# Performance work log

Hardware: AMD Instinct MI355X
Metric: run time of the kernel (lower is better)

Reference implementation:

```python
import jax, jax.numpy as jnp
import numpy as np

B, T, C, H = 4, 4096, 1024, 64

def setup_inputs() -> dict:
    key = jax.random.key(0)
    kx, kq, kk, kv = jax.random.split(key, 4)
    x  = jax.random.normal(kx, (B, T, C), dtype=jnp.float32)
    # nn.Linear(C, H, bias=False) weights have shape [H, C]; y = x @ W.T
    Wq = jax.random.normal(kq, (H, C), dtype=jnp.float32) * (C ** -0.5)
    Wk = jax.random.normal(kk, (H, C), dtype=jnp.float32) * (C ** -0.5)
    Wv = jax.random.normal(kv, (H, C), dtype=jnp.float32) * (C ** -0.5)
    return {"x": x, "Wq": Wq, "Wk": Wk, "Wv": Wv}

def reference(x, Wq, Wk, Wv):
    T_ = x.shape[1]
    scale = jnp.asarray(Wq.shape[0] ** -0.5, dtype=x.dtype)
    q = jnp.einsum('btc,hc->bth', x, Wq)
    k = jnp.einsum('btc,hc->bth', x, Wk)
    v = jnp.einsum('btc,hc->bth', x, Wv)
    w = jnp.einsum('bqh,bkh->bqk', q, k)  # [B, T, T] scores
    causal = jnp.tril(jnp.ones((T_, T_), dtype=bool))
    # original: masked_fill(-inf) then scale; -inf * scale == -inf, so equivalent
    w = jnp.where(causal, w * scale, -jnp.inf)
    w = jax.nn.softmax(w, axis=-1)
    # dropout p=0.0 (eval/deterministic): identity
    return jnp.einsum('bqk,bkh->bqh', w, v)
```

## Files before the change

kernel.cpp:

```cpp
#include <hip/hip_runtime.h>
#include <hip/hip_bf16.h>

#define B_ 4
#define T_ 4096
#define C_ 1024

typedef __bf16 bf16_t;
typedef __bf16 bf16x8 __attribute__((ext_vector_type(8)));
typedef float f32x4 __attribute__((ext_vector_type(4)));

__device__ __forceinline__ void gld16(const void* g, void* l) {
    __builtin_amdgcn_global_load_lds((const __attribute__((address_space(1))) void*)g,
                                     (__attribute__((address_space(3))) void*)l, 16, 0, 0);
}

__global__ void wcvt_kernel(const float* __restrict__ Wq, const float* __restrict__ Wk,
                            const float* __restrict__ Wv, bf16_t* __restrict__ wbf) {
    int i = blockIdx.x * 256 + threadIdx.x;
    int m = i >> 16;
    int r = i & 65535;
    const float* src = (m == 0) ? Wq : (m == 1) ? Wk : Wv;
    float s = (m == 0) ? 0.125f * 1.44269504f : 1.0f;
    wbf[i] = (bf16_t)(src[r] * s);
}

__global__ __launch_bounds__(512, 4)
void qkv_proj_kernel(const float* __restrict__ x, const bf16_t* __restrict__ wbf,
                     bf16_t* __restrict__ qb, bf16_t* __restrict__ kb,
                     bf16_t* __restrict__ vtb) {
    __shared__ float  xs[3][2048];
    __shared__ bf16_t wsb[2][12288];

    const int tid = threadIdx.x;
    const int w = tid >> 6, lane = tid & 63, lr = lane & 15, kg = lane >> 4;
    const int rg = w & 1, cg = w >> 1;
    const int row0 = blockIdx.x * 32;

    const int xr0 = tid >> 4, xu = tid & 15;
    const char* xg = (const char*)x + (size_t)(row0 + xr0) * 4096
                     + ((xu ^ (xr0 & 15)) * 16);
    const int wh = tid >> 3, wu = tid & 7;
    const char* wg = (const char*)wbf;

    char* xs_c  = (char*)&xs[0][0];
    char* xs_n  = (char*)&xs[1][0];
    char* xs_nn = (char*)&xs[2][0];
    char* ws_c  = (char*)&wsb[0][0];
    char* ws_n  = (char*)&wsb[1][0];

#define ISSUE_X(kk, dst) {                                                          \
        gld16(xg + (size_t)(kk) * 256, (dst) + (size_t)tid * 16); }
#define ISSUE_W(kk, dst) {                                                          \
        _Pragma("unroll")                                                           \
        for (int j = 0; j < 3; ++j) {                                               \
            int h = wh + j * 64;                                                    \
            gld16(wg + (size_t)h * 2048 + (size_t)(kk) * 128 + ((wu ^ (h & 7)) * 16), \
                  (dst) + (size_t)(tid + j * 512) * 16); } }

    f32x4 acc[3];
    #pragma unroll
    for (int j = 0; j < 3; ++j) acc[j] = (f32x4){0.f, 0.f, 0.f, 0.f};

    ISSUE_X(0, xs_c);
    ISSUE_W(0, ws_c);
    ISSUE_X(1, xs_n);

    const int rl = rg * 16 + lr;
    const int u00 = ((2 * kg)     ^ lr) * 16;
    const int u01 = ((2 * kg + 1) ^ lr) * 16;
    const int u10 = ((2 * kg + 8) ^ lr) * 16;
    const int u11 = ((2 * kg + 9) ^ lr) * 16;

    #pragma clang loop unroll(disable)
    for (int c = 0; c < 16; ++c) {
        if (c < 15) {
            asm volatile("s_waitcnt vmcnt(1)" ::: "memory");
        } else {
            asm volatile("s_waitcnt vmcnt(0)" ::: "memory");
        }
        __builtin_amdgcn_s_barrier();
        if (c < 15) ISSUE_W(c + 1, ws_n);
        if (c < 14) ISSUE_X(c + 2, xs_nn);

        {
            const char* xrow = xs_c + (size_t)rl * 256;
            float4 a0 = *(const float4*)(xrow + u00);
            float4 a1 = *(const float4*)(xrow + u01);
            float4 b0 = *(const float4*)(xrow + u10);
            float4 b1 = *(const float4*)(xrow + u11);
            bf16x8 af0, af1;
            af0[0]=(bf16_t)a0.x; af0[1]=(bf16_t)a0.y; af0[2]=(bf16_t)a0.z; af0[3]=(bf16_t)a0.w;
            af0[4]=(bf16_t)a1.x; af0[5]=(bf16_t)a1.y; af0[6]=(bf16_t)a1.z; af0[7]=(bf16_t)a1.w;
            af1[0]=(bf16_t)b0.x; af1[1]=(bf16_t)b0.y; af1[2]=(bf16_t)b0.z; af1[3]=(bf16_t)b0.w;
            af1[4]=(bf16_t)b1.x; af1[5]=(bf16_t)b1.y; af1[6]=(bf16_t)b1.z; af1[7]=(bf16_t)b1.w;

            __builtin_amdgcn_s_setprio(1);
            #pragma unroll
            for (int j = 0; j < 3; ++j) {
                int h = (cg * 3 + j) * 16 + lr;
                const char* wrow = ws_c + (size_t)h * 128;
                bf16x8 w0 = *(const bf16x8*)(wrow + (((kg)     ^ (lr & 7)) * 16));
                bf16x8 w1 = *(const bf16x8*)(wrow + (((kg + 4) ^ (lr & 7)) * 16));
                acc[j] = __builtin_amdgcn_mfma_f32_16x16x32_bf16(af0, w0, acc[j], 0, 0, 0);
                acc[j] = __builtin_amdgcn_mfma_f32_16x16x32_bf16(af1, w1, acc[j], 0, 0, 0);
            }
            __builtin_amdgcn_s_setprio(0);
        }

        char* tx = xs_c; xs_c = xs_n; xs_n = xs_nn; xs_nn = tx;
        char* tw = ws_c; ws_c = ws_n; ws_n = tw;
    }

    #pragma unroll
    for (int j = 0; j < 3; ++j) {
        int p = cg * 3 + j;
        int m = p >> 2;
        int h = (p & 3) * 16 + lr;
        #pragma unroll
        for (int i = 0; i < 4; ++i) {
            int t = row0 + rg * 16 + kg * 4 + i;
            float v = acc[j][i];
            if (m == 0) {
                qb[(size_t)t * 64 + h] = (bf16_t)v;
            } else if (m == 1) {
                kb[(size_t)t * 64 + ((((h >> 3) ^ (t & 7)) << 3) | (h & 7))] = (bf16_t)v;
            } else {
                int bb = t >> 12, tt = t & 4095;
                vtb[(size_t)(bb * 64 + h) * 4096 + (tt & ~63)
                    + (((((tt >> 3) & 7) ^ (h & 7))) << 3) + (tt & 7)] = (bf16_t)v;
            }
        }
    }
#undef ISSUE_X
#undef ISSUE_W
}

__global__ __launch_bounds__(256, 2)
void attn_kernel(const bf16_t* __restrict__ qb, const bf16_t* __restrict__ kb,
                 const bf16_t* __restrict__ vtb, float* __restrict__ out) {
    __shared__ bf16_t kvb[2][2][8192];
    __shared__ bf16_t p_lds[4][16][68];

    const int tid = threadIdx.x;
    const int w = tid >> 6, lane = tid & 63, lr = lane & 15, kg = lane >> 4;
    const int rg = w & 1, slice = w >> 1;
    const int bid = blockIdx.x;
    const int b = bid & 3;
    const int qt = 127 - (bid >> 2);
    const int qrow0 = qt * 32 + rg * 16;
    const size_t bT = (size_t)b * 4096;

    const int nch    = (qt + 2) >> 1;
    const int nsteps = (nch + 1) >> 1;

#define STAGE_CHUNK(kk, pp, cc) {                                                   \
        _Pragma("unroll")                                                           \
        for (int jj = 0; jj < 2; ++jj) {                                            \
            int idx = tid + jj * 256;                                               \
            gld16((const char*)kb + (bT + (size_t)(kk) * 64) * 128 + (size_t)idx * 16, \
                  (char*)&kvb[pp][cc][0] + (size_t)idx * 16);                       \
            gld16((const char*)vtb + (size_t)(b * 64 + (idx >> 3)) * 8192           \
                      + (size_t)(kk) * 128 + (idx & 7) * 16,                        \
                  (char*)&kvb[pp][cc][4096] + (size_t)idx * 16); } }
#define STAGE_PAIR(j1) {                                                            \
        int c0 = 2 * (j1), c1 = 2 * (j1) + 1, pp = (j1) & 1;                        \
        if (c0 < nch) STAGE_CHUNK(c0, pp, 0);                                       \
        if (c1 < nch) STAGE_CHUNK(c1, pp, 1); }

    bf16x8 qf[2];
    #pragma unroll
    for (int s = 0; s < 2; ++s)
        qf[s] = *(const bf16x8*)&qb[(bT + qrow0 + lr) * 64 + s * 32 + kg * 8];

    f32x4 o_acc[4];
    float l_i[4];
    #pragma unroll
    for (int ct = 0; ct < 4; ++ct) o_acc[ct] = (f32x4){0.f, 0.f, 0.f, 0.f};
    #pragma unroll
    for (int i = 0; i < 4; ++i) l_i[i] = 0.f;

    STAGE_PAIR(0);

    for (int j = 0; j < nsteps; ++j) {
        asm volatile("s_waitcnt vmcnt(0)" ::: "memory");
        __builtin_amdgcn_s_barrier();
        asm volatile("" ::: "memory");
        if (j + 1 < nsteps) STAGE_PAIR(j + 1);

        int c = 2 * j + slice;
        if (c < nch) {
            const bf16_t* Kt = &kvb[j & 1][slice][0];
            const bf16_t* Vt = &kvb[j & 1][slice][4096];
            int kv0 = c * 64;

            f32x4 sc[4];
            #pragma unroll
            for (int ct = 0; ct < 4; ++ct) sc[ct] = (f32x4){0.f, 0.f, 0.f, 0.f};
            __builtin_amdgcn_s_setprio(1);
            #pragma unroll
            for (int ct = 0; ct < 4; ++ct)
                #pragma unroll
                for (int s = 0; s < 2; ++s) {
                    bf16x8 kf = *(const bf16x8*)&Kt[(ct * 16 + lr) * 64 + (((kg + 4 * s) ^ (lr & 7)) * 8)];
                    sc[ct] = __builtin_amdgcn_mfma_f32_16x16x32_bf16(qf[s], kf, sc[ct], 0, 0, 0);
                }
            __builtin_amdgcn_s_setprio(0);

            if (kv0 + 63 > qrow0) {
                #pragma unroll
                for (int ct = 0; ct < 4; ++ct)
                    #pragma unroll
                    for (int i = 0; i < 4; ++i) {
                        int col = kv0 + ct * 16 + lr;
                        int rw  = qrow0 + kg * 4 + i;
                        if (col > rw) sc[ct][i] = -INFINITY;
                    }
            }

            #pragma unroll
            for (int ct = 0; ct < 4; ++ct)
                #pragma unroll
                for (int i = 0; i < 4; ++i) {
                    float p = __builtin_amdgcn_exp2f(sc[ct][i]);
                    p_lds[w][kg * 4 + i][ct * 16 + lr] = (bf16_t)p;
                    l_i[i] += p;
                }

            bf16x8 pf[2];
            #pragma unroll
            for (int s = 0; s < 2; ++s)
                pf[s] = *(const bf16x8*)&p_lds[w][lr][s * 32 + kg * 8];
            __builtin_amdgcn_s_setprio(1);
            #pragma unroll
            for (int ct = 0; ct < 4; ++ct)
                #pragma unroll
                for (int s = 0; s < 2; ++s) {
                    bf16x8 vf = *(const bf16x8*)&Vt[(ct * 16 + lr) * 64 + (((kg + 4 * s) ^ (lr & 7)) * 8)];
                    o_acc[ct] = __builtin_amdgcn_mfma_f32_16x16x32_bf16(pf[s], vf, o_acc[ct], 0, 0, 0);
                }
            __builtin_amdgcn_s_setprio(0);
        }
    }

    asm volatile("s_waitcnt vmcnt(0)" ::: "memory");
    __syncthreads();

    #pragma unroll
    for (int off = 1; off < 16; off <<= 1)
        #pragma unroll
        for (int i = 0; i < 4; ++i)
            l_i[i] += __shfl_xor(l_i[i], off);

    float* co = (float*)&kvb[0][0][0];
    float* cl = co + 2 * 16 * 66;
    if (slice == 1) {
        #pragma unroll
        for (int ct = 0; ct < 4; ++ct)
            #pragma unroll
            for (int i = 0; i < 4; ++i)
                co[(rg * 16 + kg * 4 + i) * 66 + ct * 16 + lr] = o_acc[ct][i];
        if (lr == 0) {
            #pragma unroll
            for (int i = 0; i < 4; ++i)
                cl[rg * 16 + kg * 4 + i] = l_i[i];
        }
    }
    __syncthreads();
    if (slice == 0) {
        #pragma unroll
        for (int i = 0; i < 4; ++i) {
            int r = kg * 4 + i;
            float lv = l_i[i] + cl[rg * 16 + r];
            float inv = 1.0f / lv;
            #pragma unroll
            for (int ct = 0; ct < 4; ++ct) {
                float ov = o_acc[ct][i] + co[(rg * 16 + r) * 66 + ct * 16 + lr];
                out[(bT + qrow0 + r) * 64 + ct * 16 + lr] = ov * inv;
            }
        }
    }
#undef STAGE_CHUNK
#undef STAGE_PAIR
}

extern "C" void kernel_launch(void* const* d_in, const int* in_sizes, int n_in,
                              void* d_out, int out_size, void* d_ws, size_t ws_size,
                              hipStream_t stream) {
    const float* x  = (const float*)d_in[0];
    const float* Wq = (const float*)d_in[1];
    const float* Wk = (const float*)d_in[2];
    const float* Wv = (const float*)d_in[3];
    float* out = (float*)d_out;

    bf16_t* ws  = (bf16_t*)d_ws;
    bf16_t* wbf = ws;
    bf16_t* qb  = ws + 196608;
    bf16_t* kb  = qb + 1048576;
    bf16_t* vtb = kb + 1048576;

    wcvt_kernel<<<768, 256, 0, stream>>>(Wq, Wk, Wv, wbf);
    qkv_proj_kernel<<<512, 512, 0, stream>>>(x, wbf, qb, kb, vtb);
    attn_kernel<<<512, 256, 0, stream>>>(qb, kb, vtb, out);
}
```

Measured before the change: 62.41 us.

## Split attention KV range four ways per 64-row query tile with separate combine kernel

The attention kernel now assigns each block a 64-row query tile (four waves of 16 rows) and one quarter of its causal KV chunk range. Each block writes partial outputs and row sums to workspace, and a new combine kernel adds the four partials and normalises. The KV staging becomes a three-buffer ring that waits on vmcnt(4), keeping one chunk in flight during compute instead of the old paired double buffer. This removes the intra-block slice reduction and evens out per-block work, at the cost of 64 MB of extra partial-output traffic and one more kernel launch.

```diff
diff --git a/kernel.cpp b/kernel.cpp
--- a/kernel.cpp
+++ b/kernel.cpp
@@ -137,40 +137,44 @@
 
 __global__ __launch_bounds__(256, 2)
 void attn_kernel(const bf16_t* __restrict__ qb, const bf16_t* __restrict__ kb,
-                 const bf16_t* __restrict__ vtb, float* __restrict__ out) {
-    __shared__ bf16_t kvb[2][2][8192];
+                 const bf16_t* __restrict__ vtb, float* __restrict__ po,
+                 float* __restrict__ pl) {
+    __shared__ bf16_t kvb[3][8192];
     __shared__ bf16_t p_lds[4][16][68];
 
     const int tid = threadIdx.x;
     const int w = tid >> 6, lane = tid & 63, lr = lane & 15, kg = lane >> 4;
-    const int rg = w & 1, slice = w >> 1;
     const int bid = blockIdx.x;
     const int b = bid & 3;
-    const int qt = 127 - (bid >> 2);
-    const int qrow0 = qt * 32 + rg * 16;
+    const int v = bid >> 2;
+    const int s = v & 3;
+    const int qt = 63 - (v >> 2);
+    const int qrow0 = qt * 64 + w * 16;
     const size_t bT = (size_t)b * 4096;
 
-    const int nch    = (qt + 2) >> 1;
-    const int nsteps = (nch + 1) >> 1;
-
-#define STAGE_CHUNK(kk, pp, cc) {                                                   \
+    const int nch   = qt + 1;
+    const int start = (nch * s) >> 2;
+    const int end   = (nch * (s + 1)) >> 2;
+    const int cnt   = end - start;
+
+    char* ks_c  = (char*)&kvb[0][0];
+    char* ks_n  = (char*)&kvb[1][0];
+    char* ks_nn = (char*)&kvb[2][0];
+
+#define STAGE_CHUNK(kk, dst) {                                                      \
         _Pragma("unroll")                                                           \
         for (int jj = 0; jj < 2; ++jj) {                                            \
             int idx = tid + jj * 256;                                               \
             gld16((const char*)kb + (bT + (size_t)(kk) * 64) * 128 + (size_t)idx * 16, \
-                  (char*)&kvb[pp][cc][0] + (size_t)idx * 16);                       \
+                  (dst) + (size_t)idx * 16);                                        \
             gld16((const char*)vtb + (size_t)(b * 64 + (idx >> 3)) * 8192           \
                       + (size_t)(kk) * 128 + (idx & 7) * 16,                        \
-                  (char*)&kvb[pp][cc][4096] + (size_t)idx * 16); } }
-#define STAGE_PAIR(j1) {                                                            \
-        int c0 = 2 * (j1), c1 = 2 * (j1) + 1, pp = (j1) & 1;                        \
-        if (c0 < nch) STAGE_CHUNK(c0, pp, 0);                                       \
-        if (c1 < nch) STAGE_CHUNK(c1, pp, 1); }
+                  (dst) + 8192 + (size_t)idx * 16); } }
 
     bf16x8 qf[2];
     #pragma unroll
-    for (int s = 0; s < 2; ++s)
-        qf[s] = *(const bf16x8*)&qb[(bT + qrow0 + lr) * 64 + s * 32 + kg * 8];
+    for (int s2 = 0; s2 < 2; ++s2)
+        qf[s2] = *(const bf16x8*)&qb[(bT + qrow0 + lr) * 64 + s2 * 32 + kg * 8];
 
     f32x4 o_acc[4];
     float l_i[4];
@@ -179,71 +183,73 @@
     #pragma unroll
     for (int i = 0; i < 4; ++i) l_i[i] = 0.f;
 
-    STAGE_PAIR(0);
-
-    for (int j = 0; j < nsteps; ++j) {
-        asm volatile("s_waitcnt vmcnt(0)" ::: "memory");
+    if (cnt > 0) STAGE_CHUNK(start, ks_c);
+    if (cnt > 1) STAGE_CHUNK(start + 1, ks_n);
+
+    for (int j = 0; j < cnt; ++j) {
+        if (j < cnt - 1) {
+            asm volatile("s_waitcnt vmcnt(4)" ::: "memory");
+        } else {
+            asm volatile("s_waitcnt vmcnt(0)" ::: "memory");
+        }
         __builtin_amdgcn_s_barrier();
         asm volatile("" ::: "memory");
-        if (j + 1 < nsteps) STAGE_PAIR(j + 1);
-
-        int c = 2 * j + slice;
-        if (c < nch) {
-            const bf16_t* Kt = &kvb[j & 1][slice][0];
-            const bf16_t* Vt = &kvb[j & 1][slice][4096];
-            int kv0 = c * 64;
-
-            f32x4 sc[4];
-            #pragma unroll
-            for (int ct = 0; ct < 4; ++ct) sc[ct] = (f32x4){0.f, 0.f, 0.f, 0.f};
-            __builtin_amdgcn_s_setprio(1);
-            #pragma unroll
-            for (int ct = 0; ct < 4; ++ct)
-                #pragma unroll
-                for (int s = 0; s < 2; ++s) {
-                    bf16x8 kf = *(const bf16x8*)&Kt[(ct * 16 + lr) * 64 + (((kg + 4 * s) ^ (lr & 7)) * 8)];
-                    sc[ct] = __builtin_amdgcn_mfma_f32_16x16x32_bf16(qf[s], kf, sc[ct], 0, 0, 0);
-                }
-            __builtin_amdgcn_s_setprio(0);
-
-            if (kv0 + 63 > qrow0) {
-                #pragma unroll
-                for (int ct = 0; ct < 4; ++ct)
-                    #pragma unroll
-                    for (int i = 0; i < 4; ++i) {
-                        int col = kv0 + ct * 16 + lr;
-                        int rw  = qrow0 + kg * 4 + i;
-                        if (col > rw) sc[ct][i] = -INFINITY;
-                    }
-            }
-
+        if (j + 2 < cnt) STAGE_CHUNK(start + j + 2, ks_nn);
+
+        const bf16_t* Kt = (const bf16_t*)ks_c;
+        const bf16_t* Vt = (const bf16_t*)(ks_c + 8192);
+        const int c = start + j;
+        const int kv0 = c * 64;
+
+        f32x4 sc[4];
+        #pragma unroll
+        for (int ct = 0; ct < 4; ++ct) sc[ct] = (f32x4){0.f, 0.f, 0.f, 0.f};
+        __builtin_amdgcn_s_setprio(1);
+        #pragma unroll
+        for (int ct = 0; ct < 4; ++ct)
+            #pragma unroll
+            for (int s2 = 0; s2 < 2; ++s2) {
+                bf16x8 kf = *(const bf16x8*)&Kt[(ct * 16 + lr) * 64 + (((kg + 4 * s2) ^ (lr & 7)) * 8)];
+                sc[ct] = __builtin_amdgcn_mfma_f32_16x16x32_bf16(qf[s2], kf, sc[ct], 0, 0, 0);
+            }
+        __builtin_amdgcn_s_setprio(0);
+
+        if (c == nch - 1) {
             #pragma unroll
             for (int ct = 0; ct < 4; ++ct)
                 #pragma unroll
                 for (int i = 0; i < 4; ++i) {
-                    float p = __builtin_amdgcn_exp2f(sc[ct][i]);
-                    p_lds[w][kg * 4 + i][ct * 16 + lr] = (bf16_t)p;
-                    l_i[i] += p;
+                    int col = kv0 + ct * 16 + lr;
+                    int rw  = qrow0 + kg * 4 + i;
+                    if (col > rw) sc[ct][i] = -INFINITY;
                 }
-
-            bf16x8 pf[2];
-            #pragma unroll
-            for (int s = 0; s < 2; ++s)
-                pf[s] = *(const bf16x8*)&p_lds[w][lr][s * 32 + kg * 8];
-            __builtin_amdgcn_s_setprio(1);
-            #pragma unroll
-            for (int ct = 0; ct < 4; ++ct)
-                #pragma unroll
-                for (int s = 0; s < 2; ++s) {
-                    bf16x8 vf = *(const bf16x8*)&Vt[(ct * 16 + lr) * 64 + (((kg + 4 * s) ^ (lr & 7)) * 8)];
-                    o_acc[ct] = __builtin_amdgcn_mfma_f32_16x16x32_bf16(pf[s], vf, o_acc[ct], 0, 0, 0);
-                }
-            __builtin_amdgcn_s_setprio(0);
-        }
+        }
+
+        #pragma unroll
+        for (int ct = 0; ct < 4; ++ct)
+            #pragma unroll
+            for (int i = 0; i < 4; ++i) {
+                float p = __builtin_amdgcn_exp2f(sc[ct][i]);
+                p_lds[w][kg * 4 + i][ct * 16 + lr] = (bf16_t)p;
+                l_i[i] += p;
+            }
+
+        bf16x8 pf[2];
+        #pragma unroll
+        for (int s2 = 0; s2 < 2; ++s2)
+            pf[s2] = *(const bf16x8*)&p_lds[w][lr][s2 * 32 + kg * 8];
+        __builtin_amdgcn_s_setprio(1);
+        #pragma unroll
+        for (int ct = 0; ct < 4; ++ct)
+            #pragma unroll
+            for (int s2 = 0; s2 < 2; ++s2) {
+                bf16x8 vf = *(const bf16x8*)&Vt[(ct * 16 + lr) * 64 + (((kg + 4 * s2) ^ (lr & 7)) * 8)];
+                o_acc[ct] = __builtin_amdgcn_mfma_f32_16x16x32_bf16(pf[s2], vf, o_acc[ct], 0, 0, 0);
+            }
+        __builtin_amdgcn_s_setprio(0);
+
+        char* t0 = ks_c; ks_c = ks_n; ks_n = ks_nn; ks_nn = t0;
     }
-
-    asm volatile("s_waitcnt vmcnt(0)" ::: "memory");
-    __syncthreads();
 
     #pragma unroll
     for (int off = 1; off < 16; off <<= 1)
@@ -251,36 +257,27 @@
         for (int i = 0; i < 4; ++i)
             l_i[i] += __shfl_xor(l_i[i], off);
 
-    float* co = (float*)&kvb[0][0][0];
-    float* cl = co + 2 * 16 * 66;
-    if (slice == 1) {
+    const size_t pbase = ((size_t)s * 4 + b) * 4096;
+    #pragma unroll
+    for (int i = 0; i < 4; ++i) {
+        int row = qt * 64 + w * 16 + kg * 4 + i;
         #pragma unroll
         for (int ct = 0; ct < 4; ++ct)
-            #pragma unroll
-            for (int i = 0; i < 4; ++i)
-                co[(rg * 16 + kg * 4 + i) * 66 + ct * 16 + lr] = o_acc[ct][i];
-        if (lr == 0) {
-            #pragma unroll
-            for (int i = 0; i < 4; ++i)
-                cl[rg * 16 + kg * 4 + i] = l_i[i];
-        }
-    }
-    __syncthreads();
-    if (slice == 0) {
-        #pragma unroll
-        for (int i = 0; i < 4; ++i) {
-            int r = kg * 4 + i;
-            float lv = l_i[i] + cl[rg * 16 + r];
-            float inv = 1.0f / lv;
-            #pragma unroll
-            for (int ct = 0; ct < 4; ++ct) {
-                float ov = o_acc[ct][i] + co[(rg * 16 + r) * 66 + ct * 16 + lr];
-                out[(bT + qrow0 + r) * 64 + ct * 16 + lr] = ov * inv;
-            }
-        }
+            po[(pbase + row) * 64 + ct * 16 + lr] = o_acc[ct][i];
+        if (lr == 0) pl[pbase + row] = l_i[i];
     }
 #undef STAGE_CHUNK
-#undef STAGE_PAIR
+}
+
+__global__ __launch_bounds__(256)
+void combine_kernel(const float* __restrict__ po, const float* __restrict__ pl,
+                    float* __restrict__ out) {
+    int idx = blockIdx.x * 256 + threadIdx.x;
+    int row = idx >> 4;
+    const f32x4* p4 = (const f32x4*)po;
+    f32x4 vsum = p4[idx] + p4[262144 + idx] + p4[2 * 262144 + idx] + p4[3 * 262144 + idx];
+    float l = pl[row] + pl[16384 + row] + pl[32768 + row] + pl[49152 + row];
+    ((f32x4*)out)[idx] = vsum * (1.0f / l);
 }
 
 extern "C" void kernel_launch(void* const* d_in, const int* in_sizes, int n_in,
@@ -297,8 +294,11 @@
     bf16_t* qb  = ws + 196608;
     bf16_t* kb  = qb + 1048576;
     bf16_t* vtb = kb + 1048576;
+    float*  po  = (float*)(vtb + 1048576);
+    float*  pl  = po + 4 * 1048576;
 
     wcvt_kernel<<<768, 256, 0, stream>>>(Wq, Wk, Wv, wbf);
     qkv_proj_kernel<<<512, 512, 0, stream>>>(x, wbf, qb, kb, vtb);
-    attn_kernel<<<512, 256, 0, stream>>>(qb, kb, vtb, out);
-}
+    attn_kernel<<<1024, 256, 0, stream>>>(qb, kb, vtb, po, pl);
+    combine_kernel<<<1024, 256, 0, stream>>>(po, pl, out);
+}
```

New measurement: 56.02 us (median of 2 runs). -10.2%, faster.
